# Kernel optimization log

Measured on AMD Instinct MI355X. Metric: run time of the kernel, lower is better.

Reference implementation:

```python
import jax, jax.numpy as jnp
import numpy as np

C = 64  # in_dim

def _dwpw(x, w_dw, w_pw):
    # depthwise 1x1x1 conv (groups=C, no bias) == per-channel scale
    x = x * w_dw[None, :, None, None, None]
    # pointwise 1x1x1 conv (no bias) == channel mixing matmul
    return jnp.einsum('bcdhw,oc->bodhw', x, w_pw)

def setup_inputs() -> dict:
    key = jax.random.key(0)
    ks = jax.random.split(key, 8)
    B, D, H, W = 2, 16, 16, 16
    x = jax.random.normal(ks[0], (B, C, D, H, W), dtype=jnp.float32)
    s = 1.0 / np.sqrt(C)
    q_dw = jax.random.normal(ks[1], (C,), dtype=jnp.float32) * s
    q_pw = jax.random.normal(ks[2], (C, C), dtype=jnp.float32) * s
    k_dw = jax.random.normal(ks[3], (C,), dtype=jnp.float32) * s
    k_pw = jax.random.normal(ks[4], (C, C), dtype=jnp.float32) * s
    v_dw = jax.random.normal(ks[5], (C,), dtype=jnp.float32) * s
    v_pw = jax.random.normal(ks[6], (C, C), dtype=jnp.float32) * s
    gamma = jnp.zeros((1,), dtype=jnp.float32) + 0.1  # nonzero so output depends on attention
    return {"x": x, "q_dw": q_dw, "q_pw": q_pw, "k_dw": k_dw, "k_pw": k_pw,
            "v_dw": v_dw, "v_pw": v_pw, "gamma": gamma}

def reference(x, q_dw, q_pw, k_dw, k_pw, v_dw, v_pw, gamma):
    B, Cc, D, H, W = x.shape
    N = D * H * W
    q = _dwpw(x, q_dw, q_pw).reshape(B, Cc, N)  # [B,C,N]
    k = _dwpw(x, k_dw, k_pw).reshape(B, Cc, N)
    v = _dwpw(x, v_dw, v_pw).reshape(B, Cc, N)
    # energy[b,i,j] = sum_c q[b,c,i] * k[b,c,j]
    energy = jnp.einsum('bci,bcj->bij', q, k)
    attn = jax.nn.softmax(energy, axis=-1)  # softmax over j
    # out[b,c,i] = sum_j v[b,c,j] * attn[b,i,j]
    out = jnp.einsum('bcj,bij->bci', v, attn).reshape(B, Cc, D, H, W)
    return gamma * out + x
```

## Files before the change

kernel.cpp:

```cpp
#include <hip/hip_runtime.h>
#include <hip/hip_bf16.h>

#define NPOS 4096
#define CDIM 64
#define BATCH 2
#define JSPLIT 16
#define JCHUNK (NPOS / JSPLIT)
#define RPB 128
#define PSTR 72
#define WSTR 72

typedef __attribute__((ext_vector_type(8))) short bf16x8;
typedef __attribute__((ext_vector_type(4))) float f32x4;
typedef __attribute__((ext_vector_type(4))) unsigned int u32x4;
typedef __attribute__((ext_vector_type(2))) unsigned int u32x2;

static __device__ __forceinline__ unsigned int fbits(float f) {
    union { float f; unsigned int u; } v; v.f = f; return v.u;
}
static __device__ __forceinline__ float bffloat(unsigned int hi16) {
    union { unsigned int u; float f; } v; v.u = hi16; return v.f;
}
static __device__ __forceinline__ unsigned int pk2bf(float a, float b) {
    return ((fbits(a) + 0x8000u) >> 16) | ((fbits(b) + 0x8000u) & 0xffff0000u);
}
static __device__ __forceinline__ short f2bs(float f) {
    return (short)(unsigned short)((fbits(f) + 0x8000u) >> 16);
}

__global__ __launch_bounds__(256) void qkv_kernel(
    const float* __restrict__ x,
    const float* __restrict__ q_dw, const float* __restrict__ q_pw,
    const float* __restrict__ k_dw, const float* __restrict__ k_pw,
    const float* __restrict__ v_dw, const float* __restrict__ v_pw,
    short* __restrict__ qT, short* __restrict__ kT, short* __restrict__ vM)
{
    int b  = blockIdx.x >> 6;
    int n0 = (blockIdx.x & 63) << 6;

    __shared__ __align__(16) short Wbf[192 * WSTR];

    int t = threadIdx.x;
    for (int i = t; i < 192 * 64; i += 256) {
        int op = i >> 6, c = i & 63, p = op >> 6, o = op & 63;
        const float* pw = (p == 0) ? q_pw : (p == 1) ? k_pw : v_pw;
        const float* dw = (p == 0) ? q_dw : (p == 1) ? k_dw : v_dw;
        Wbf[op * WSTR + c] = f2bs(pw[o * 64 + c] * dw[c]);
    }
    __syncthreads();

    const int wave = t >> 6, lane = t & 63, col = lane & 15, quad = lane >> 4;
    const int n = n0 + wave * 16 + col;

    bf16x8 xf0, xf1;
    #pragma unroll
    for (int j = 0; j < 8; ++j) {
        xf0[j] = f2bs(x[(size_t)(b * CDIM + quad * 8 + j) * NPOS + n]);
        xf1[j] = f2bs(x[(size_t)(b * CDIM + 32 + quad * 8 + j) * NPOS + n]);
    }

    #pragma unroll
    for (int p = 0; p < 2; ++p) {
        short* dst = (p == 0) ? qT : kT;
        #pragma unroll
        for (int os = 0; os < 4; ++os) {
            const short* wp = Wbf + (p * 64 + os * 16 + col) * WSTR + quad * 8;
            bf16x8 wf0 = *(const bf16x8*)wp;
            bf16x8 wf1 = *(const bf16x8*)(wp + 32);
            f32x4 d = (f32x4){0.f, 0.f, 0.f, 0.f};
            d = __builtin_amdgcn_mfma_f32_16x16x32_bf16(wf0, xf0, d, 0, 0, 0);
            d = __builtin_amdgcn_mfma_f32_16x16x32_bf16(wf1, xf1, d, 0, 0, 0);
            *(u32x2*)(dst + (size_t)(b * NPOS + n) * CDIM + os * 16 + quad * 4) =
                (u32x2){pk2bf(d[0], d[1]), pk2bf(d[2], d[3])};
        }
    }
    #pragma unroll
    for (int os = 0; os < 4; ++os) {
        const short* wp = Wbf + (128 + os * 16 + col) * WSTR + quad * 8;
        bf16x8 wf0 = *(const bf16x8*)wp;
        bf16x8 wf1 = *(const bf16x8*)(wp + 32);
        f32x4 d = (f32x4){0.f, 0.f, 0.f, 0.f};
        d = __builtin_amdgcn_mfma_f32_16x16x32_bf16(xf0, wf0, d, 0, 0, 0);
        d = __builtin_amdgcn_mfma_f32_16x16x32_bf16(xf1, wf1, d, 0, 0, 0);
        *(u32x2*)(vM + (size_t)(b * CDIM + os * 16 + col) * NPOS + n0 + wave * 16 + quad * 4) =
            (u32x2){pk2bf(d[0], d[1]), pk2bf(d[2], d[3])};
    }
}

__global__ __launch_bounds__(256) void attn_kernel(
    const short* __restrict__ qT, const short* __restrict__ kT,
    const short* __restrict__ vM,
    unsigned short* __restrict__ Opart, float* __restrict__ lacc)
{
    const int gid  = blockIdx.x;
    const int jc   = gid & (JSPLIT - 1);
    const int rb   = (gid >> 4) & 31;
    const int b    = gid >> 9;
    const int t    = threadIdx.x;
    const int wave = t >> 6;
    const int lane = t & 63;
    const int col  = lane & 15;
    const int quad = lane >> 4;

    __shared__ __align__(16) short Pw[4][32 * PSTR];

    const short* qTb = qT + (size_t)b * NPOS * CDIM;
    const short* kTb = kT + (size_t)b * NPOS * CDIM;
    const short* vb  = vM + (size_t)b * CDIM * NPOS;

    const int i0 = rb * RPB + wave * 32;

    bf16x8 qf[2][2];
    #pragma unroll
    for (int rs = 0; rs < 2; ++rs) {
        const short* qp = qTb + (size_t)(i0 + rs * 16 + col) * CDIM + quad * 8;
        qf[rs][0] = *(const bf16x8*)qp;
        qf[rs][1] = *(const bf16x8*)(qp + 32);
    }

    f32x4 oacc[2][4];
    #pragma unroll
    for (int rs = 0; rs < 2; ++rs)
        #pragma unroll
        for (int cb = 0; cb < 4; ++cb) oacc[rs][cb] = (f32x4){0.f, 0.f, 0.f, 0.f};
    float lp[2] = {0.f, 0.f};

    short* Pme = Pw[wave];

    for (int jt = 0; jt < JCHUNK / 64; ++jt) {
        const int j0 = jc * JCHUNK + jt * 64;

        #pragma unroll
        for (int ct = 0; ct < 4; ++ct) {
            const short* kp = kTb + (size_t)(j0 + ct * 16 + col) * CDIM + quad * 8;
            bf16x8 kf0 = *(const bf16x8*)kp;
            bf16x8 kf1 = *(const bf16x8*)(kp + 32);
            #pragma unroll
            for (int rs = 0; rs < 2; ++rs) {
                f32x4 a = (f32x4){0.f, 0.f, 0.f, 0.f};
                a = __builtin_amdgcn_mfma_f32_16x16x32_bf16(kf0, qf[rs][0], a, 0, 0, 0);
                a = __builtin_amdgcn_mfma_f32_16x16x32_bf16(kf1, qf[rs][1], a, 0, 0, 0);
                float p0 = __expf(a[0]), p1 = __expf(a[1]);
                float p2 = __expf(a[2]), p3 = __expf(a[3]);
                lp[rs] += (p0 + p1) + (p2 + p3);
                *(u32x2*)(Pme + (rs * 16 + col) * PSTR + ct * 16 + quad * 4) =
                    (u32x2){pk2bf(p0, p1), pk2bf(p2, p3)};
            }
        }
        __syncthreads();

        bf16x8 pf[2][2];
        #pragma unroll
        for (int rs = 0; rs < 2; ++rs) {
            const short* pp = Pme + (rs * 16 + col) * PSTR + quad * 8;
            pf[rs][0] = *(const bf16x8*)pp;
            pf[rs][1] = *(const bf16x8*)(pp + 32);
        }

        #pragma unroll
        for (int cb = 0; cb < 4; ++cb) {
            const short* vp = vb + (size_t)(cb * 16 + col) * NPOS + j0 + quad * 8;
            bf16x8 vf0 = *(const bf16x8*)vp;
            bf16x8 vf1 = *(const bf16x8*)(vp + 32);
            #pragma unroll
            for (int rs = 0; rs < 2; ++rs) {
                oacc[rs][cb] = __builtin_amdgcn_mfma_f32_16x16x32_bf16(vf0, pf[rs][0], oacc[rs][cb], 0, 0, 0);
                oacc[rs][cb] = __builtin_amdgcn_mfma_f32_16x16x32_bf16(vf1, pf[rs][1], oacc[rs][cb], 0, 0, 0);
            }
        }
        __syncthreads();
    }

    #pragma unroll
    for (int rs = 0; rs < 2; ++rs) {
        lp[rs] += __shfl_xor(lp[rs], 16, 64);
        lp[rs] += __shfl_xor(lp[rs], 32, 64);
    }
    if (quad == 0) {
        #pragma unroll
        for (int rs = 0; rs < 2; ++rs)
            lacc[(size_t)(jc * BATCH + b) * NPOS + i0 + rs * 16 + col] = lp[rs];
    }

    unsigned short* Ob = Opart + (size_t)(jc * BATCH + b) * CDIM * NPOS;
    #pragma unroll
    for (int rs = 0; rs < 2; ++rs)
        #pragma unroll
        for (int cb = 0; cb < 4; ++cb)
            #pragma unroll
            for (int r = 0; r < 4; ++r)
                Ob[(size_t)(cb * 16 + quad * 4 + r) * NPOS + i0 + rs * 16 + col] =
                    (unsigned short)f2bs(oacc[rs][cb][r]);
}

__global__ __launch_bounds__(256) void combine_kernel(
    const unsigned short* __restrict__ Opart, const float* __restrict__ lacc,
    const float* __restrict__ x, const float* __restrict__ gamma,
    float* __restrict__ out)
{
    int b  = blockIdx.x >> 6;
    int n0 = (blockIdx.x & 63) << 6;
    __shared__ float linv[64];
    int t = threadIdx.x;
    if (t < 64) {
        float s = 0.f;
        #pragma unroll
        for (int jc = 0; jc < JSPLIT; ++jc)
            s += lacc[(size_t)(jc * BATCH + b) * NPOS + n0 + t];
        linv[t] = gamma[0] / s;
    }
    __syncthreads();

    int c = t >> 2, ns = (t & 3) * 16;
    float acc[16];
    #pragma unroll
    for (int k = 0; k < 16; ++k) acc[k] = 0.f;
    #pragma unroll
    for (int jc = 0; jc < JSPLIT; ++jc) {
        const unsigned short* Ob = Opart + ((size_t)(jc * BATCH + b) * CDIM + c) * NPOS + n0 + ns;
        #pragma unroll
        for (int h = 0; h < 2; ++h) {
            u32x4 w = *(const u32x4*)(Ob + h * 8);
            #pragma unroll
            for (int j = 0; j < 4; ++j) {
                acc[h * 8 + 2 * j]     += bffloat(w[j] << 16);
                acc[h * 8 + 2 * j + 1] += bffloat(w[j] & 0xffff0000u);
            }
        }
    }
    const float* xb = x + ((size_t)b * CDIM + c) * NPOS + n0 + ns;
    float* ob = out + ((size_t)b * CDIM + c) * NPOS + n0 + ns;
    #pragma unroll
    for (int k = 0; k < 4; ++k) {
        f32x4 x4 = *(const f32x4*)(xb + k * 4);
        f32x4 r;
        #pragma unroll
        for (int j = 0; j < 4; ++j)
            r[j] = fmaf(acc[k * 4 + j], linv[ns + k * 4 + j], x4[j]);
        *(f32x4*)(ob + k * 4) = r;
    }
}

extern "C" void kernel_launch(void* const* d_in, const int* in_sizes, int n_in,
                              void* d_out, int out_size, void* d_ws, size_t ws_size,
                              hipStream_t stream) {
    const float* x     = (const float*)d_in[0];
    const float* q_dw  = (const float*)d_in[1];
    const float* q_pw  = (const float*)d_in[2];
    const float* k_dw  = (const float*)d_in[3];
    const float* k_pw  = (const float*)d_in[4];
    const float* v_dw  = (const float*)d_in[5];
    const float* v_pw  = (const float*)d_in[6];
    const float* gamma = (const float*)d_in[7];
    float* out = (float*)d_out;

    char* ws = (char*)d_ws;
    short* qT             = (short*)(ws);
    short* kT             = (short*)(ws + (1u << 20));
    short* vM             = (short*)(ws + (2u << 20));
    unsigned short* Opart = (unsigned short*)(ws + (3u << 20));
    float* lacc           = (float*)(ws + (3u << 20) +
                                     (size_t)JSPLIT * BATCH * CDIM * NPOS * 2);

    qkv_kernel<<<BATCH * 64, 256, 0, stream>>>(
        x, q_dw, q_pw, k_dw, k_pw, v_dw, v_pw, qT, kT, vM);
    attn_kernel<<<BATCH * 32 * JSPLIT, 256, 0, stream>>>(qT, kT, vM, Opart, lacc);
    combine_kernel<<<BATCH * 64, 256, 0, stream>>>(Opart, lacc, x, gamma, out);
}
```

Before: 121.6 us.

## Precompute fused QKV weights once and split projection into more small blocks

Moves the depthwise-times-pointwise weight fusion and bf16 conversion into a separate small kernel that writes the weights to workspace once, instead of having every projection block rebuild them in shared memory. The projection kernel becomes 1536 single-wave blocks, each handling one of q/k/v for 16 positions, so the grid covers more CUs with less redundant per-block setup. It adds a kernel launch and has each block read weights from global memory (likely L2-resident). The x tile is now loaded three times, once per projection.

```diff
diff --git a/kernel.cpp b/kernel.cpp
--- a/kernel.cpp
+++ b/kernel.cpp
@@ -8,7 +8,6 @@
 #define JCHUNK (NPOS / JSPLIT)
 #define RPB 128
 #define PSTR 72
-#define WSTR 72
 
 typedef __attribute__((ext_vector_type(8))) short bf16x8;
 typedef __attribute__((ext_vector_type(4))) float f32x4;
@@ -28,29 +27,33 @@
     return (short)(unsigned short)((fbits(f) + 0x8000u) >> 16);
 }
 
-__global__ __launch_bounds__(256) void qkv_kernel(
-    const float* __restrict__ x,
+__global__ __launch_bounds__(256) void weff_kernel(
     const float* __restrict__ q_dw, const float* __restrict__ q_pw,
     const float* __restrict__ k_dw, const float* __restrict__ k_pw,
     const float* __restrict__ v_dw, const float* __restrict__ v_pw,
+    short* __restrict__ Wg)
+{
+    int i = blockIdx.x * 256 + threadIdx.x;
+    if (i >= 192 * 64) return;
+    int op = i >> 6, c = i & 63, p = op >> 6, o = op & 63;
+    const float* pw = (p == 0) ? q_pw : (p == 1) ? k_pw : v_pw;
+    const float* dw = (p == 0) ? q_dw : (p == 1) ? k_dw : v_dw;
+    Wg[i] = f2bs(pw[o * 64 + c] * dw[c]);
+}
+
+__global__ __launch_bounds__(64) void qkv_kernel(
+    const float* __restrict__ x, const short* __restrict__ Wg,
     short* __restrict__ qT, short* __restrict__ kT, short* __restrict__ vM)
 {
-    int b  = blockIdx.x >> 6;
-    int n0 = (blockIdx.x & 63) << 6;
-
-    __shared__ __align__(16) short Wbf[192 * WSTR];
-
-    int t = threadIdx.x;
-    for (int i = t; i < 192 * 64; i += 256) {
-        int op = i >> 6, c = i & 63, p = op >> 6, o = op & 63;
-        const float* pw = (p == 0) ? q_pw : (p == 1) ? k_pw : v_pw;
-        const float* dw = (p == 0) ? q_dw : (p == 1) ? k_dw : v_dw;
-        Wbf[op * WSTR + c] = f2bs(pw[o * 64 + c] * dw[c]);
-    }
-    __syncthreads();
-
-    const int wave = t >> 6, lane = t & 63, col = lane & 15, quad = lane >> 4;
-    const int n = n0 + wave * 16 + col;
+    const int bid  = blockIdx.x;
+    const int p    = bid >> 9;
+    const int np   = bid & 511;
+    const int b    = np >> 8;
+    const int n0   = (np & 255) << 4;
+    const int lane = threadIdx.x;
+    const int col  = lane & 15;
+    const int quad = lane >> 4;
+    const int n    = n0 + col;
 
     bf16x8 xf0, xf1;
     #pragma unroll
@@ -59,12 +62,11 @@
         xf1[j] = f2bs(x[(size_t)(b * CDIM + 32 + quad * 8 + j) * NPOS + n]);
     }
 
-    #pragma unroll
-    for (int p = 0; p < 2; ++p) {
-        short* dst = (p == 0) ? qT : kT;
+    if (p < 2) {
+        short* dst = p ? kT : qT;
         #pragma unroll
         for (int os = 0; os < 4; ++os) {
-            const short* wp = Wbf + (p * 64 + os * 16 + col) * WSTR + quad * 8;
+            const short* wp = Wg + (p * 64 + os * 16 + col) * 64 + quad * 8;
             bf16x8 wf0 = *(const bf16x8*)wp;
             bf16x8 wf1 = *(const bf16x8*)(wp + 32);
             f32x4 d = (f32x4){0.f, 0.f, 0.f, 0.f};
@@ -73,17 +75,18 @@
             *(u32x2*)(dst + (size_t)(b * NPOS + n) * CDIM + os * 16 + quad * 4) =
                 (u32x2){pk2bf(d[0], d[1]), pk2bf(d[2], d[3])};
         }
-    }
-    #pragma unroll
-    for (int os = 0; os < 4; ++os) {
-        const short* wp = Wbf + (128 + os * 16 + col) * WSTR + quad * 8;
-        bf16x8 wf0 = *(const bf16x8*)wp;
-        bf16x8 wf1 = *(const bf16x8*)(wp + 32);
-        f32x4 d = (f32x4){0.f, 0.f, 0.f, 0.f};
-        d = __builtin_amdgcn_mfma_f32_16x16x32_bf16(xf0, wf0, d, 0, 0, 0);
-        d = __builtin_amdgcn_mfma_f32_16x16x32_bf16(xf1, wf1, d, 0, 0, 0);
-        *(u32x2*)(vM + (size_t)(b * CDIM + os * 16 + col) * NPOS + n0 + wave * 16 + quad * 4) =
-            (u32x2){pk2bf(d[0], d[1]), pk2bf(d[2], d[3])};
+    } else {
+        #pragma unroll
+        for (int os = 0; os < 4; ++os) {
+            const short* wp = Wg + (128 + os * 16 + col) * 64 + quad * 8;
+            bf16x8 wf0 = *(const bf16x8*)wp;
+            bf16x8 wf1 = *(const bf16x8*)(wp + 32);
+            f32x4 d = (f32x4){0.f, 0.f, 0.f, 0.f};
+            d = __builtin_amdgcn_mfma_f32_16x16x32_bf16(xf0, wf0, d, 0, 0, 0);
+            d = __builtin_amdgcn_mfma_f32_16x16x32_bf16(xf1, wf1, d, 0, 0, 0);
+            *(u32x2*)(vM + (size_t)(b * CDIM + os * 16 + col) * NPOS + n0 + quad * 4) =
+                (u32x2){pk2bf(d[0], d[1]), pk2bf(d[2], d[3])};
+        }
     }
 }
 
@@ -258,12 +261,13 @@
     short* qT             = (short*)(ws);
     short* kT             = (short*)(ws + (1u << 20));
     short* vM             = (short*)(ws + (2u << 20));
-    unsigned short* Opart = (unsigned short*)(ws + (3u << 20));
-    float* lacc           = (float*)(ws + (3u << 20) +
+    short* Wg             = (short*)(ws + (3u << 20));
+    unsigned short* Opart = (unsigned short*)(ws + (3u << 20) + (1u << 16));
+    float* lacc           = (float*)(ws + (3u << 20) + (1u << 16) +
                                      (size_t)JSPLIT * BATCH * CDIM * NPOS * 2);
 
-    qkv_kernel<<<BATCH * 64, 256, 0, stream>>>(
-        x, q_dw, q_pw, k_dw, k_pw, v_dw, v_pw, qT, kT, vM);
+    weff_kernel<<<48, 256, 0, stream>>>(q_dw, q_pw, k_dw, k_pw, v_dw, v_pw, Wg);
+    qkv_kernel<<<3 * BATCH * 256, 64, 0, stream>>>(x, Wg, qT, kT, vM);
     attn_kernel<<<BATCH * 32 * JSPLIT, 256, 0, stream>>>(qT, kT, vM, Opart, lacc);
     combine_kernel<<<BATCH * 64, 256, 0, stream>>>(Opart, lacc, x, gamma, out);
 }
```

After: 120.6 us. About the same (-0.8%).
